# Kernel tuning notes

Hardware: AMD Instinct MI355X
Metric: run time of the kernel (lower is better)

Reference implementation:

```python
import jax, jax.numpy as jnp
import numpy as np

B, T, C = 2, 2048, 1024
N_HEAD = 16
HEAD_DIM = C // N_HEAD


def setup_inputs() -> dict:
    key = jax.random.key(0)
    k1, k2, k3 = jax.random.split(key, 3)
    x = jax.random.normal(k1, (B, T, C), dtype=jnp.float32)
    w_attn = jax.random.normal(k2, (C, 3 * C), dtype=jnp.float32) * 0.02
    b_attn = jnp.zeros((3 * C,), dtype=jnp.float32)
    w_proj = jax.random.normal(k3, (C, C), dtype=jnp.float32) * 0.02
    b_proj = jnp.zeros((C,), dtype=jnp.float32)
    return {"x": x, "w_attn": w_attn, "b_attn": b_attn, "w_proj": w_proj, "b_proj": b_proj}


def reference(x, w_attn, b_attn, w_proj, b_proj):
    Bz, Tz, Cz = x.shape
    qkv = x @ w_attn + b_attn                       # [B, T, 3C]
    q, k, v = jnp.split(qkv, 3, axis=-1)
    # [B, H, T, D]
    q = q.reshape(Bz, Tz, N_HEAD, HEAD_DIM).transpose(0, 2, 1, 3)
    k = k.reshape(Bz, Tz, N_HEAD, HEAD_DIM).transpose(0, 2, 1, 3)
    v = v.reshape(Bz, Tz, N_HEAD, HEAD_DIM).transpose(0, 2, 1, 3)
    scale = 1.0 / np.sqrt(HEAD_DIM).astype(np.float32)
    att = jnp.einsum('bhqd,bhkd->bhqk', q, k) * scale  # [B, H, T, T]
    causal = jnp.tril(jnp.ones((Tz, Tz), dtype=bool))
    att = jnp.where(causal[None, None], att, -jnp.inf)
    att = jax.nn.softmax(att, axis=-1)
    y = jnp.einsum('bhqk,bhkd->bhqd', att, v)          # [B, H, T, D]
    y = y.transpose(0, 2, 1, 3).reshape(Bz, Tz, Cz)
    return y @ w_proj + b_proj
```

## Files before the change

kernel.cpp:

```cpp
#include <hip/hip_runtime.h>
#include <stdint.h>

#define T_SEQ 2048
#define NH 16
#define HD 64
#define M_DIM 4096
#define K_DIM 1024

typedef __attribute__((ext_vector_type(8))) short bf16x8;
typedef __attribute__((ext_vector_type(4))) short bf16x4;
typedef __attribute__((ext_vector_type(4))) float f32x4;
typedef __attribute__((ext_vector_type(4))) unsigned short u16x4;

__device__ __forceinline__ unsigned short f2bf(float f) {
  union { float f; uint32_t u; } x; x.f = f;
  uint32_t u = x.u;
  return (unsigned short)((u + 0x7fffu + ((u >> 16) & 1u)) >> 16);
}

__device__ __forceinline__ uint32_t cvtpk_bf16(float a, float b) {
  uint32_t r;
  asm("v_cvt_pk_bf16_f32 %0, %1, %2" : "=v"(r) : "v"(a), "v"(b));
  return r;
}

__device__ __forceinline__ f32x4 mfma16(bf16x4 a, bf16x4 b, f32x4 c) {
  asm("v_mfma_f32_16x16x16_bf16 %0, %1, %2, %0" : "+v"(c) : "v"(a), "v"(b));
  return c;
}

#define GLOAD16(g, l) __builtin_amdgcn_global_load_lds( \
    (const __attribute__((address_space(1))) unsigned int*)(g), \
    (__attribute__((address_space(3))) unsigned int*)(l), 16, 0, 0)

__device__ __forceinline__ void do_convert(const float* __restrict__ src,
                                           unsigned short* __restrict__ dst, int bid) {
  int idx = (bid * 256 + threadIdx.x) * 4;
  f32x4 v = *(const f32x4*)(src + idx);
  u16x4 o;
  #pragma unroll
  for (int i = 0; i < 4; ++i) o[i] = f2bf(v[i]);
  *(u16x4*)(dst + idx) = o;
}

__device__ __forceinline__ void do_transpose(const float* __restrict__ src,
                                             unsigned short* __restrict__ dst,
                                             int R, int Cn, int bx, int by,
                                             float (*tile)[65]) {
  const int r0 = by * 64, c0 = bx * 64;
  const int t = threadIdx.x;
  const int rr = t >> 4;
  const int c4 = (t & 15) * 4;
  #pragma unroll
  for (int p = 0; p < 4; ++p) {
    f32x4 v = *(const f32x4*)(src + (size_t)(r0 + p * 16 + rr) * Cn + c0 + c4);
    #pragma unroll
    for (int i = 0; i < 4; ++i) tile[p * 16 + rr][c4 + i] = v[i];
  }
  __syncthreads();
  #pragma unroll
  for (int p = 0; p < 4; ++p) {
    const int cl = p * 16 + rr;
    u16x4 o;
    #pragma unroll
    for (int i = 0; i < 4; ++i) o[i] = f2bf(tile[c4 + i][cl]);
    *(u16x4*)(dst + (size_t)(c0 + cl) * R + r0 + c4) = o;
  }
}

__global__ __launch_bounds__(256) void prep_kernel(
    const float* __restrict__ x, unsigned short* __restrict__ xb,
    const float* __restrict__ w_attn, unsigned short* __restrict__ wqkvT,
    const float* __restrict__ w_proj, unsigned short* __restrict__ wprojT) {
  __shared__ float tile[64][65];
  const int b = blockIdx.x;
  if (b < 4096) {
    do_convert(x, xb, b);
  } else if (b < 4096 + 768) {
    const int bid = b - 4096;
    do_transpose(w_attn, wqkvT, 1024, 3072, bid % 48, bid / 48, tile);
  } else {
    const int bid = b - 4864;
    do_transpose(w_proj, wprojT, 1024, 1024, bid % 16, bid / 16, tile);
  }
}

template <int MODE>
__global__ __launch_bounds__(256, 3) void gemm3_kernel(
    const unsigned short* __restrict__ A,
    const unsigned short* __restrict__ Bt,
    const float* __restrict__ bias,
    unsigned short* __restrict__ qout,
    unsigned short* __restrict__ kout,
    unsigned short* __restrict__ vTout,
    float* __restrict__ fout) {
  constexpr int NS = K_DIM / 32;
  constexpr int NWG = (MODE == 0) ? 768 : 256;
  constexpr int NBC = (MODE == 0) ? 24 : 8;
  __shared__ __align__(16) unsigned short As[3][128 * 32];
  __shared__ __align__(16) unsigned short Bs[3][128 * 32];
  const int t = threadIdx.x;
  const int w = t >> 6, l = t & 63;
  const int wr = w >> 1, wc = w & 1;
  const int lr = l & 15, lg = l >> 4;
  const int wg = (blockIdx.x & 7) * (NWG >> 3) + (blockIdx.x >> 3);
  const int bc = wg % NBC, br = wg / NBC;

  f32x4 acc[4][4];
  const f32x4 zf = {0.f, 0.f, 0.f, 0.f};
  #pragma unroll
  for (int i = 0; i < 4; ++i)
    #pragma unroll
    for (int j = 0; j < 4; ++j) acc[i][j] = zf;

  const unsigned short* Abase = A + (size_t)(br * 128) * K_DIM;
  const unsigned short* Bbase = Bt + (size_t)(bc * 128) * K_DIM;
  const int uA0 = t, uA1 = t + 256;
  const int uB0 = t, uB1 = t + 256;

  #define STAGE(ks, buf) do {                                                   \
    const int k0 = (ks) * 32;                                                   \
    unsigned short* as = &As[0][0] + (buf) * (128 * 32);                        \
    unsigned short* bs = &Bs[0][0] + (buf) * (128 * 32);                        \
    GLOAD16(Abase + (size_t)(uA0 >> 2) * K_DIM + k0 + (uA0 & 3) * 8, as + uA0 * 8); \
    GLOAD16(Abase + (size_t)(uA1 >> 2) * K_DIM + k0 + (uA1 & 3) * 8, as + uA1 * 8); \
    GLOAD16(Bbase + (size_t)(uB0 >> 2) * K_DIM + k0 + (uB0 & 3) * 8, bs + uB0 * 8); \
    GLOAD16(Bbase + (size_t)(uB1 >> 2) * K_DIM + k0 + (uB1 & 3) * 8, bs + uB1 * 8); \
  } while (0)

  #define COMPUTE(buf) do {                                                      \
    const unsigned short* as = &As[0][0] + (buf) * (128 * 32);                   \
    const unsigned short* bs = &Bs[0][0] + (buf) * (128 * 32);                   \
    bf16x8 af[4], bfv[4];                                                        \
    _Pragma("unroll")                                                            \
    for (int f = 0; f < 4; ++f) {                                                \
      af[f]  = *(const bf16x8*)(as + (wr * 64 + f * 16 + lr) * 32 + lg * 8);     \
      bfv[f] = *(const bf16x8*)(bs + (wc * 64 + f * 16 + lr) * 32 + lg * 8);     \
    }                                                                            \
    _Pragma("unroll")                                                            \
    for (int fr = 0; fr < 4; ++fr)                                               \
      _Pragma("unroll")                                                          \
      for (int fc = 0; fc < 4; ++fc)                                             \
        acc[fr][fc] = __builtin_amdgcn_mfma_f32_16x16x32_bf16(af[fr], bfv[fc],   \
                                                              acc[fr][fc], 0, 0, 0); \
  } while (0)

  STAGE(0, 0);
  STAGE(1, 1);
  int b_cur = 0;
  #pragma unroll 1
  for (int ks = 0; ks < NS; ++ks) {
    if (ks == NS - 1) {
      asm volatile("s_waitcnt vmcnt(0)" ::: "memory");
    } else {
      asm volatile("s_waitcnt vmcnt(4)" ::: "memory");
    }
    __builtin_amdgcn_sched_barrier(0);
    __builtin_amdgcn_s_barrier();
    if (ks + 2 < NS) {
      const int b_stg = (b_cur == 0) ? 2 : b_cur - 1;
      STAGE(ks + 2, b_stg);
    }
    COMPUTE(b_cur);
    b_cur = (b_cur == 2) ? 0 : b_cur + 1;
  }
  #undef STAGE
  #undef COMPUTE

  #pragma unroll
  for (int fr = 0; fr < 4; ++fr) {
    #pragma unroll
    for (int fc = 0; fc < 4; ++fc) {
      const int m0 = br * 128 + wr * 64 + fr * 16 + lg * 4;
      const int n  = bc * 128 + wc * 64 + fc * 16 + lr;
      if (MODE == 0) {
        const int which = n >> 10, rem = n & 1023;
        const int h = rem >> 6, d = rem & 63;
        const int b = m0 >> 11, tt0 = m0 & 2047;
        const int bh = b * NH + h;
        if (which == 2) {
          u16x4 pack;
          #pragma unroll
          for (int r = 0; r < 4; ++r) pack[r] = f2bf(acc[fr][fc][r] + bias[n]);
          *(u16x4*)(vTout + ((size_t)bh * HD + d) * T_SEQ + tt0) = pack;
        } else {
          unsigned short* o = (which == 0) ? qout : kout;
          const float sc = (which == 0) ? 0.18033688011112042f : 1.0f;
          #pragma unroll
          for (int r = 0; r < 4; ++r)
            o[((size_t)bh * T_SEQ + tt0 + r) * HD + d] = f2bf((acc[fr][fc][r] + bias[n]) * sc);
        }
      } else {
        #pragma unroll
        for (int r = 0; r < 4; ++r)
          fout[(size_t)(m0 + r) * 1024 + n] = acc[fr][fc][r] + bias[n];
      }
    }
  }
}

__global__ __launch_bounds__(256, 4) void flash_attn_kernel(
    const unsigned short* __restrict__ qg,
    const unsigned short* __restrict__ kg,
    const unsigned short* __restrict__ vTg,
    unsigned short* __restrict__ yg) {
  __shared__ __align__(16) unsigned short Ks[2][64 * 64];
  __shared__ __align__(16) unsigned short Vs[2][64 * 64];

  const int t = threadIdx.x;
  const int w = t >> 6, l = t & 63;
  const int lr = l & 15, lg = l >> 4;
  const int i = blockIdx.x;
  const int bh = (i & 7) * 4 + ((i >> 3) & 3);
  const int qt = 31 - (i >> 5);
  const int nt = qt + 1;
  const int qw = qt * 64 + w * 16;
  const int qrow = qw + lr;
  const int swz = lr & 7;

  const int srow0 = t >> 3;
  const int sch = t & 7;

  const size_t kgb = (size_t)bh * T_SEQ * HD;
  const size_t vgb = (size_t)bh * HD * T_SEQ;
  const f32x4 zf = {0.f, 0.f, 0.f, 0.f};

  const size_t qoff = ((size_t)bh * T_SEQ + qw + lr) * HD + lg * 8;
  const bf16x8 qf0 = *(const bf16x8*)(qg + qoff);
  const bf16x8 qf1 = *(const bf16x8*)(qg + qoff + 32);

  f32x4 acc[4];
  #pragma unroll
  for (int k = 0; k < 4; ++k) acc[k] = zf;
  float m_run = 0.f;
  float l_part = 0.f;

  #pragma unroll
  for (int sh = 0; sh < 2; ++sh) {
    const int row = sh * 32 + srow0;
    const int sc = (sch ^ (row & 7)) * 8;
    GLOAD16(kg + kgb + (size_t)row * HD + sc, Ks[0] + row * 64 + sch * 8);
    GLOAD16(vTg + vgb + (size_t)row * T_SEQ + sc, Vs[0] + row * 64 + sch * 8);
  }
  __syncthreads();

  int cur = 0;
  #pragma unroll 1
  for (int it = 0; it < nt; ++it) {
    const int kv0 = it * 64;
    if (it + 1 < nt) {
      const int kvn = kv0 + 64;
      #pragma unroll
      for (int sh = 0; sh < 2; ++sh) {
        const int row = sh * 32 + srow0;
        const int sc = (sch ^ (row & 7)) * 8;
        GLOAD16(kg + kgb + (size_t)(kvn + row) * HD + sc, Ks[cur ^ 1] + row * 64 + sch * 8);
        GLOAD16(vTg + vgb + (size_t)row * T_SEQ + kvn + sc, Vs[cur ^ 1] + row * 64 + sch * 8);
      }
    }

    f32x4 s[4];
    __builtin_amdgcn_s_setprio(1);
    #pragma unroll
    for (int fc = 0; fc < 4; ++fc) {
      const unsigned short* kr = Ks[cur] + (fc * 16 + lr) * 64;
      const bf16x8 k0v = *(const bf16x8*)(kr + ((lg ^ swz) * 8));
      const bf16x8 k1v = *(const bf16x8*)(kr + (((lg + 4) ^ swz) * 8));
      f32x4 sv = zf;
      sv = __builtin_amdgcn_mfma_f32_16x16x32_bf16(k0v, qf0, sv, 0, 0, 0);
      sv = __builtin_amdgcn_mfma_f32_16x16x32_bf16(k1v, qf1, sv, 0, 0, 0);
      s[fc] = sv;
    }
    __builtin_amdgcn_s_setprio(0);

    if (it == nt - 1) {
      #pragma unroll
      for (int fc = 0; fc < 4; ++fc)
        #pragma unroll
        for (int r = 0; r < 4; ++r) {
          const int tkv = kv0 + fc * 16 + lg * 4 + r;
          if (tkv > qrow) s[fc][r] = -1e30f;
        }
    }

    float mt = s[0][0];
    #pragma unroll
    for (int fc = 0; fc < 4; ++fc)
      #pragma unroll
      for (int r = 0; r < 4; ++r) mt = fmaxf(mt, s[fc][r]);
    if (__any(mt > m_run + 8.f)) {
      float mrow = fmaxf(mt, __shfl_xor(mt, 16));
      mrow = fmaxf(mrow, __shfl_xor(mrow, 32));
      const float m_new = fmaxf(m_run, mrow);
      const float fac = __builtin_amdgcn_exp2f(m_run - m_new);
      l_part *= fac;
      float frs[4];
      #pragma unroll
      for (int r = 0; r < 4; ++r) frs[r] = __shfl(fac, lg * 4 + r);
      #pragma unroll
      for (int fd = 0; fd < 4; ++fd)
        #pragma unroll
        for (int r = 0; r < 4; ++r) acc[fd][r] *= frs[r];
      m_run = m_new;
    }

    union { uint32_t d[2]; bf16x4 v; } pkd[4];
    #pragma unroll
    for (int fc = 0; fc < 4; ++fc) {
      float e0 = __builtin_amdgcn_exp2f(s[fc][0] - m_run);
      float e1 = __builtin_amdgcn_exp2f(s[fc][1] - m_run);
      float e2 = __builtin_amdgcn_exp2f(s[fc][2] - m_run);
      float e3 = __builtin_amdgcn_exp2f(s[fc][3] - m_run);
      l_part += (e0 + e1) + (e2 + e3);
      pkd[fc].d[0] = cvtpk_bf16(e0, e1);
      pkd[fc].d[1] = cvtpk_bf16(e2, e3);
    }

    __builtin_amdgcn_s_setprio(1);
    #pragma unroll
    for (int fd = 0; fd < 4; ++fd) {
      const unsigned short* vr = Vs[cur] + (fd * 16 + lr) * 64;
      bf16x4 vf[4];
      #pragma unroll
      for (int fc = 0; fc < 4; ++fc) {
        const int ch = (fc * 2 + (lg >> 1)) ^ swz;
        vf[fc] = *(const bf16x4*)(vr + ch * 8 + (lg & 1) * 4);
      }
      f32x4 a = acc[fd];
      #pragma unroll
      for (int fc = 0; fc < 4; ++fc) a = mfma16(pkd[fc].v, vf[fc], a);
      acc[fd] = a;
    }
    __builtin_amdgcn_s_setprio(0);
    __syncthreads();
    cur ^= 1;
  }

  float lsum = l_part;
  lsum += __shfl_xor(lsum, 16);
  lsum += __shfl_xor(lsum, 32);

  const int b = bh >> 4, h = bh & 15;
  #pragma unroll
  for (int r = 0; r < 4; ++r) {
    const float lv = __shfl(lsum, lg * 4 + r);
    const float linv = 1.f / lv;
    const int tt = qw + lg * 4 + r;
    #pragma unroll
    for (int fd = 0; fd < 4; ++fd) {
      const int d = fd * 16 + lr;
      yg[(((size_t)b * T_SEQ + tt) * NH + h) * HD + d] = f2bf(acc[fd][r] * linv);
    }
  }
}

extern "C" void kernel_launch(void* const* d_in, const int* in_sizes, int n_in,
                              void* d_out, int out_size, void* d_ws, size_t ws_size,
                              hipStream_t stream) {
  (void)in_sizes; (void)n_in; (void)out_size; (void)ws_size;
  const float* x      = (const float*)d_in[0];
  const float* w_attn = (const float*)d_in[1];
  const float* b_attn = (const float*)d_in[2];
  const float* w_proj = (const float*)d_in[3];
  const float* b_proj = (const float*)d_in[4];
  float* out = (float*)d_out;

  char* ws = (char*)d_ws;
  unsigned short* xb     = (unsigned short*)(ws);
  unsigned short* wqkvT  = (unsigned short*)(ws + (8ull  << 20));
  unsigned short* wprojT = (unsigned short*)(ws + (14ull << 20));
  unsigned short* qb     = (unsigned short*)(ws + (16ull << 20));
  unsigned short* kb     = (unsigned short*)(ws + (24ull << 20));
  unsigned short* vT     = (unsigned short*)(ws + (32ull << 20));
  unsigned short* yb     = (unsigned short*)(ws + (40ull << 20));

  prep_kernel<<<5120, 256, 0, stream>>>(x, xb, w_attn, wqkvT, w_proj, wprojT);
  gemm3_kernel<0><<<768, 256, 0, stream>>>(xb, wqkvT, b_attn, qb, kb, vT, nullptr);
  flash_attn_kernel<<<1024, 256, 0, stream>>>(qb, kb, vT, yb);
  gemm3_kernel<1><<<256, 256, 0, stream>>>(yb, wprojT, b_proj, nullptr, nullptr, nullptr, out);
}
```

Baseline: 179.9 us.

## Triple-buffer K/V tiles with two-ahead prefetch and one barrier per iteration

Moves the flash attention K/V staging from double to triple buffering. Each iteration waits on vmcnt for its tile, takes one barrier, then issues the load for tile it+2, which removes the trailing __syncthreads. Also computes the row max with 3-input max chains and skips the m_run subtraction in exp2 until the first rescale. LDS per block grows from 32KB to 48KB and launch bounds drop to 3 blocks per CU, lowering occupancy.

New measurement: 180.6 us. Within noise of the previous version (+0.4%).

```diff
diff --git a/kernel.cpp b/kernel.cpp
--- a/kernel.cpp
+++ b/kernel.cpp
@@ -27,6 +27,10 @@
 __device__ __forceinline__ f32x4 mfma16(bf16x4 a, bf16x4 b, f32x4 c) {
   asm("v_mfma_f32_16x16x16_bf16 %0, %1, %2, %0" : "+v"(c) : "v"(a), "v"(b));
   return c;
+}
+
+__device__ __forceinline__ float max3f(float a, float b, float c) {
+  return fmaxf(fmaxf(a, b), c);
 }
 
 #define GLOAD16(g, l) __builtin_amdgcn_global_load_lds( \
@@ -199,13 +203,13 @@
   }
 }
 
-__global__ __launch_bounds__(256, 4) void flash_attn_kernel(
+__global__ __launch_bounds__(256, 3) void flash_attn_kernel(
     const unsigned short* __restrict__ qg,
     const unsigned short* __restrict__ kg,
     const unsigned short* __restrict__ vTg,
     unsigned short* __restrict__ yg) {
-  __shared__ __align__(16) unsigned short Ks[2][64 * 64];
-  __shared__ __align__(16) unsigned short Vs[2][64 * 64];
+  __shared__ __align__(16) unsigned short Ks[3][64 * 64];
+  __shared__ __align__(16) unsigned short Vs[3][64 * 64];
 
   const int t = threadIdx.x;
   const int w = t >> 6, l = t & 63;
@@ -234,31 +238,39 @@
   for (int k = 0; k < 4; ++k) acc[k] = zf;
   float m_run = 0.f;
   float l_part = 0.f;
-
-  #pragma unroll
-  for (int sh = 0; sh < 2; ++sh) {
-    const int row = sh * 32 + srow0;
-    const int sc = (sch ^ (row & 7)) * 8;
-    GLOAD16(kg + kgb + (size_t)row * HD + sc, Ks[0] + row * 64 + sch * 8);
-    GLOAD16(vTg + vgb + (size_t)row * T_SEQ + sc, Vs[0] + row * 64 + sch * 8);
-  }
-  __syncthreads();
+  bool rescaled = false;
+
+  #define FSTAGE(kvt, buf) do {                                                  \
+    const size_t kof = kgb + (size_t)(kvt) * 64 * HD;                            \
+    const size_t vof = vgb + (size_t)(kvt) * 64;                                 \
+    _Pragma("unroll")                                                            \
+    for (int sh = 0; sh < 2; ++sh) {                                             \
+      const int row = sh * 32 + srow0;                                           \
+      const int sc = (sch ^ (row & 7)) * 8;                                      \
+      GLOAD16(kg + kof + (size_t)row * HD + sc, Ks[buf] + row * 64 + sch * 8);   \
+      GLOAD16(vTg + vof + (size_t)row * T_SEQ + sc, Vs[buf] + row * 64 + sch * 8); \
+    }                                                                            \
+  } while (0)
+
+  FSTAGE(0, 0);
+  if (nt > 1) FSTAGE(1, 1);
 
   int cur = 0;
   #pragma unroll 1
   for (int it = 0; it < nt; ++it) {
+    if (it == nt - 1) {
+      asm volatile("s_waitcnt vmcnt(0)" ::: "memory");
+    } else {
+      asm volatile("s_waitcnt vmcnt(4)" ::: "memory");
+    }
+    __builtin_amdgcn_sched_barrier(0);
+    __builtin_amdgcn_s_barrier();
+    if (it + 2 < nt) {
+      const int b_stg = (cur == 0) ? 2 : cur - 1;
+      FSTAGE(it + 2, b_stg);
+    }
+
     const int kv0 = it * 64;
-    if (it + 1 < nt) {
-      const int kvn = kv0 + 64;
-      #pragma unroll
-      for (int sh = 0; sh < 2; ++sh) {
-        const int row = sh * 32 + srow0;
-        const int sc = (sch ^ (row & 7)) * 8;
-        GLOAD16(kg + kgb + (size_t)(kvn + row) * HD + sc, Ks[cur ^ 1] + row * 64 + sch * 8);
-        GLOAD16(vTg + vgb + (size_t)row * T_SEQ + kvn + sc, Vs[cur ^ 1] + row * 64 + sch * 8);
-      }
-    }
-
     f32x4 s[4];
     __builtin_amdgcn_s_setprio(1);
     #pragma unroll
@@ -283,11 +295,14 @@
         }
     }
 
-    float mt = s[0][0];
-    #pragma unroll
-    for (int fc = 0; fc < 4; ++fc)
-      #pragma unroll
-      for (int r = 0; r < 4; ++r) mt = fmaxf(mt, s[fc][r]);
+    float mt = max3f(s[0][0], s[0][1], s[0][2]);
+    mt = max3f(mt, s[0][3], s[1][0]);
+    mt = max3f(mt, s[1][1], s[1][2]);
+    mt = max3f(mt, s[1][3], s[2][0]);
+    mt = max3f(mt, s[2][1], s[2][2]);
+    mt = max3f(mt, s[2][3], s[3][0]);
+    mt = max3f(mt, s[3][1], s[3][2]);
+    mt = fmaxf(mt, s[3][3]);
     if (__any(mt > m_run + 8.f)) {
       float mrow = fmaxf(mt, __shfl_xor(mt, 16));
       mrow = fmaxf(mrow, __shfl_xor(mrow, 32));
@@ -302,19 +317,33 @@
         #pragma unroll
         for (int r = 0; r < 4; ++r) acc[fd][r] *= frs[r];
       m_run = m_new;
-    }
-
+      rescaled = true;
+    }
+
+    float e[4][4];
+    if (rescaled) {
+      #pragma unroll
+      for (int fc = 0; fc < 4; ++fc)
+        #pragma unroll
+        for (int r = 0; r < 4; ++r)
+          e[fc][r] = __builtin_amdgcn_exp2f(s[fc][r] - m_run);
+    } else {
+      #pragma unroll
+      for (int fc = 0; fc < 4; ++fc)
+        #pragma unroll
+        for (int r = 0; r < 4; ++r)
+          e[fc][r] = __builtin_amdgcn_exp2f(s[fc][r]);
+    }
     union { uint32_t d[2]; bf16x4 v; } pkd[4];
     #pragma unroll
     for (int fc = 0; fc < 4; ++fc) {
-      float e0 = __builtin_amdgcn_exp2f(s[fc][0] - m_run);
-      float e1 = __builtin_amdgcn_exp2f(s[fc][1] - m_run);
-      float e2 = __builtin_amdgcn_exp2f(s[fc][2] - m_run);
-      float e3 = __builtin_amdgcn_exp2f(s[fc][3] - m_run);
-      l_part += (e0 + e1) + (e2 + e3);
-      pkd[fc].d[0] = cvtpk_bf16(e0, e1);
-      pkd[fc].d[1] = cvtpk_bf16(e2, e3);
-    }
+      pkd[fc].d[0] = cvtpk_bf16(e[fc][0], e[fc][1]);
+      pkd[fc].d[1] = cvtpk_bf16(e[fc][2], e[fc][3]);
+    }
+    l_part += (((e[0][0] + e[0][1]) + (e[0][2] + e[0][3])) +
+               ((e[1][0] + e[1][1]) + (e[1][2] + e[1][3]))) +
+              (((e[2][0] + e[2][1]) + (e[2][2] + e[2][3])) +
+               ((e[3][0] + e[3][1]) + (e[3][2] + e[3][3])));
 
     __builtin_amdgcn_s_setprio(1);
     #pragma unroll
@@ -332,9 +361,9 @@
       acc[fd] = a;
     }
     __builtin_amdgcn_s_setprio(0);
-    __syncthreads();
-    cur ^= 1;
-  }
+    cur = (cur == 2) ? 0 : cur + 1;
+  }
+  #undef FSTAGE
 
   float lsum = l_part;
   lsum += __shfl_xor(lsum, 16);
```
